# Performance work log

Hardware: AMD Instinct MI355X
Metric: run time of the kernel (lower is better)

Reference implementation:

```python
import jax, jax.numpy as jnp
import numpy as np

BATCH_BMM = 4      # opt.batch_size // len(opt.gpu_ids)
EPS = 1.0          # opt.eps (Sinkhorn entropic regularization)
MAX_ITER = 50
_STAB = 1e-8


def _cost_matrix_cos(x, y):
    # x: [B, n, d], y: [B, m, d] -> C = 1 - cosine similarity, [B, n, m]
    xn = x / (jnp.linalg.norm(x, axis=-1, keepdims=True) + _STAB)
    yn = y / (jnp.linalg.norm(y, axis=-1, keepdims=True) + _STAB)
    return 1.0 - jnp.einsum('bnd,bmd->bnm', xn, yn)


def _sinkhorn_plan(C, eps, max_iter):
    # Standard Sinkhorn with uniform marginals; returns transport plan pi [B, n, m]
    B, n, m = C.shape
    mu = jnp.full((B, n), 1.0 / n, dtype=C.dtype)
    nu = jnp.full((B, m), 1.0 / m, dtype=C.dtype)
    K = jnp.exp(-C / eps)  # Gibbs kernel, kept resident across iterations

    def body(carry, _):
        u, v = carry
        u = mu / (jnp.einsum('bnm,bm->bn', K, v) + _STAB)
        v = nu / (jnp.einsum('bnm,bn->bm', K, u) + _STAB)
        return (u, v), None

    (u, v), _ = jax.lax.scan(body, (jnp.ones_like(mu), jnp.ones_like(nu)),
                             None, length=max_iter)
    return u[:, :, None] * K * v[:, None, :]


def _OT(x, y, eps=EPS, max_iter=MAX_ITER):
    return _sinkhorn_plan(_cost_matrix_cos(x, y), eps, max_iter)


def setup_inputs() -> dict:
    key = jax.random.key(0)
    k1, k2, k3 = jax.random.split(key, 3)
    N, D = 8192, 256  # B*num_patches, feature dim
    return {
        'feat_src': jax.random.normal(k1, (N, D), dtype=jnp.float32),
        'feat_tgt': jax.random.normal(k2, (N, D), dtype=jnp.float32),
        'feat_gen': jax.random.normal(k3, (N, D), dtype=jnp.float32),
    }


def reference(feat_src, feat_tgt, feat_gen):
    dim = feat_src.shape[1]
    # .view(batch_dim_for_bmm, -1, dim); src/tgt are detached in the original
    ot_src = jax.lax.stop_gradient(feat_src.reshape(BATCH_BMM, -1, dim))
    ot_tgt = jax.lax.stop_gradient(feat_tgt.reshape(BATCH_BMM, -1, dim))
    ot_gen = feat_gen.reshape(BATCH_BMM, -1, dim)
    f1 = _OT(ot_src, ot_tgt)  # [B, n, n]
    f2 = _OT(ot_tgt, ot_gen)  # [B, n, n]
    return jnp.mean(jnp.abs(f1 - f2))  # F.l1_loss, reduction='mean'
```

## Files before the change

kernel.cpp:

```cpp
#include <hip/hip_runtime.h>
#include <math.h>

#define NP 2048
#define DF 256
#define NPROB 8
#define NTOT 8192

constexpr float F_MU   = 1.0f / 2048.0f;
constexpr float F_STAB = 1e-8f;

constexpr size_t OFF_K   = 0;
constexpr size_t SZ_K    = (size_t)NPROB * NP * NP;
constexpr size_t OFF_VA  = OFF_K + SZ_K;
constexpr size_t SZ_VA   = (size_t)3 * NPROB * NP;
constexpr size_t OFF_U   = OFF_VA + SZ_VA;
constexpr size_t SZ_U    = (size_t)NPROB * NP;
constexpr size_t OFF_INV = OFF_U + SZ_U;
constexpr size_t SZ_INV  = (size_t)3 * NTOT;
constexpr size_t OFF_SUM = OFF_INV + SZ_INV;

__global__ __launch_bounds__(256) void k_norms(const float* __restrict__ src,
                                               const float* __restrict__ tgt,
                                               const float* __restrict__ gen,
                                               float* __restrict__ inv) {
    int gw   = (blockIdx.x * 256 + threadIdx.x) >> 6;
    int lane = threadIdx.x & 63;
    int a = gw >> 13;
    int r = gw & 8191;
    const float* base = (a == 0 ? src : (a == 1 ? tgt : gen)) + (size_t)r * DF;
    float4 x = reinterpret_cast<const float4*>(base)[lane];
    float s = x.x * x.x + x.y * x.y + x.z * x.z + x.w * x.w;
    #pragma unroll
    for (int off = 32; off; off >>= 1) s += __shfl_xor(s, off);
    if (lane == 0) inv[gw] = 1.0f / (sqrtf(s) + F_STAB);
}

__global__ void k_init(float* __restrict__ va0, float* __restrict__ sum) {
    int i = blockIdx.x * 256 + threadIdx.x;
    if (i < NPROB * NP) va0[i] = 0.0f;
    if (i == 0) sum[0] = 0.0f;
}

#define TK 16
__global__ __launch_bounds__(256) void k_build(const float* __restrict__ src,
                                               const float* __restrict__ tgt,
                                               const float* __restrict__ gen,
                                               const float* __restrict__ inv,
                                               float* __restrict__ K) {
    __shared__ float As[128][TK + 1];
    __shared__ float Bs[128][TK + 1];
    int bid = blockIdx.x;
    int p   = bid >> 8;
    int t   = bid & 255;
    int ti  = t >> 4, tj = t & 15;
    int ot  = p >> 2, b = p & 3;
    const float* X    = (ot == 0) ? src : tgt;
    const float* Y    = (ot == 0) ? tgt : gen;
    const float* invx = inv + (ot == 0 ? 0 : NTOT);
    const float* invy = inv + (ot == 0 ? NTOT : 2 * NTOT);
    int rowA0 = b * NP + ti * 128;
    int rowB0 = b * NP + tj * 128;

    int tid = threadIdx.x;
    int ty  = tid >> 4, tx = tid & 15;

    float acc[8][8];
    #pragma unroll
    for (int i = 0; i < 8; ++i)
        #pragma unroll
        for (int j = 0; j < 8; ++j) acc[i][j] = 0.0f;

    for (int kb = 0; kb < DF; kb += TK) {
        __syncthreads();
        #pragma unroll
        for (int s = 0; s < 2; ++s) {
            int j4  = tid + s * 256;
            int row = j4 >> 2;
            int c4  = (j4 & 3) * 4;
            float4 av = *reinterpret_cast<const float4*>(X + (size_t)(rowA0 + row) * DF + kb + c4);
            float  sa = invx[rowA0 + row];
            As[row][c4 + 0] = av.x * sa; As[row][c4 + 1] = av.y * sa;
            As[row][c4 + 2] = av.z * sa; As[row][c4 + 3] = av.w * sa;
            float4 bv = *reinterpret_cast<const float4*>(Y + (size_t)(rowB0 + row) * DF + kb + c4);
            float  sb = invy[rowB0 + row];
            Bs[row][c4 + 0] = bv.x * sb; Bs[row][c4 + 1] = bv.y * sb;
            Bs[row][c4 + 2] = bv.z * sb; Bs[row][c4 + 3] = bv.w * sb;
        }
        __syncthreads();
        #pragma unroll
        for (int kk = 0; kk < TK; ++kk) {
            float a[8], bb[8];
            #pragma unroll
            for (int i = 0; i < 8; ++i) a[i]  = As[ty + 16 * i][kk];
            #pragma unroll
            for (int j = 0; j < 8; ++j) bb[j] = Bs[tx + 16 * j][kk];
            #pragma unroll
            for (int i = 0; i < 8; ++i)
                #pragma unroll
                for (int j = 0; j < 8; ++j) acc[i][j] += a[i] * bb[j];
        }
    }

    float* Kp = K + (size_t)p * NP * NP;
    #pragma unroll
    for (int i = 0; i < 8; ++i) {
        int gi = ti * 128 + ty + 16 * i;
        #pragma unroll
        for (int j = 0; j < 8; ++j) {
            int gj = tj * 128 + tx + 16 * j;
            Kp[(size_t)gi * NP + gj] = expf(acc[i][j] - 1.0f);
        }
    }
}

__global__ __launch_bounds__(256) void k_sink(const float* __restrict__ K,
                                              float* __restrict__ u,
                                              const float* __restrict__ vR,
                                              float* __restrict__ vW,
                                              float* __restrict__ vZ,
                                              int first) {
    __shared__ float lds[4][NP];
    int bid  = blockIdx.x;
    int p    = bid >> 6;
    int blk  = bid & 63;
    int tid  = threadIdx.x;
    int w    = tid >> 6, lane = tid & 63;

    if (tid < 32) vZ[bid * 32 + tid] = 0.0f;

    float4 vr[8];
    if (first) {
        #pragma unroll
        for (int c = 0; c < 8; ++c) vr[c] = make_float4(1.f, 1.f, 1.f, 1.f);
    } else {
        const float4* vRp = reinterpret_cast<const float4*>(vR + (size_t)p * NP);
        #pragma unroll
        for (int c = 0; c < 8; ++c) {
            float4 r4 = vRp[c * 64 + lane];
            vr[c] = make_float4(F_MU / (r4.x + F_STAB), F_MU / (r4.y + F_STAB),
                                F_MU / (r4.z + F_STAB), F_MU / (r4.w + F_STAB));
        }
    }

    const float* Kp = K + (size_t)p * NP * NP;
    float4 va[8];
    #pragma unroll
    for (int c = 0; c < 8; ++c) va[c] = make_float4(0.f, 0.f, 0.f, 0.f);

    int row0 = blk * 32 + w * 8;
    for (int r = 0; r < 8; ++r) {
        int row = row0 + r;
        const float4* krow = reinterpret_cast<const float4*>(Kp + (size_t)row * NP);
        float4 k4[8];
        #pragma unroll
        for (int c = 0; c < 8; ++c) k4[c] = krow[c * 64 + lane];
        float d = 0.f;
        #pragma unroll
        for (int c = 0; c < 8; ++c)
            d += k4[c].x * vr[c].x + k4[c].y * vr[c].y + k4[c].z * vr[c].z + k4[c].w * vr[c].w;
        #pragma unroll
        for (int off = 32; off; off >>= 1) d += __shfl_xor(d, off);
        float ui = F_MU / (d + F_STAB);
        if (lane == 0) u[p * NP + row] = ui;
        #pragma unroll
        for (int c = 0; c < 8; ++c) {
            va[c].x += k4[c].x * ui; va[c].y += k4[c].y * ui;
            va[c].z += k4[c].z * ui; va[c].w += k4[c].w * ui;
        }
    }

    float4* lw = reinterpret_cast<float4*>(lds[w]);
    #pragma unroll
    for (int c = 0; c < 8; ++c) lw[c * 64 + lane] = va[c];
    __syncthreads();
    float* vWp = vW + (size_t)p * NP;
    const float4* l0 = reinterpret_cast<const float4*>(lds[0]);
    const float4* l1 = reinterpret_cast<const float4*>(lds[1]);
    const float4* l2 = reinterpret_cast<const float4*>(lds[2]);
    const float4* l3 = reinterpret_cast<const float4*>(lds[3]);
    #pragma unroll
    for (int s = 0; s < 2; ++s) {
        int j = tid + s * 256;
        float4 a0 = l0[j], a1 = l1[j], a2 = l2[j], a3 = l3[j];
        atomicAdd(&vWp[4 * j + 0], a0.x + a1.x + a2.x + a3.x);
        atomicAdd(&vWp[4 * j + 1], a0.y + a1.y + a2.y + a3.y);
        atomicAdd(&vWp[4 * j + 2], a0.z + a1.z + a2.z + a3.z);
        atomicAdd(&vWp[4 * j + 3], a0.w + a1.w + a2.w + a3.w);
    }
}

__global__ __launch_bounds__(256) void k_freduce(const float* __restrict__ K,
                                                 const float* __restrict__ u,
                                                 const float* __restrict__ vF,
                                                 float* __restrict__ sum) {
    int bid = blockIdx.x;
    int b   = bid >> 6;
    int blk = bid & 63;
    int tid = threadIdx.x;
    int w   = tid >> 6, lane = tid & 63;
    int p1 = b, p2 = 4 + b;

    float4 v1[8], v2[8];
    const float4* vF1 = reinterpret_cast<const float4*>(vF + (size_t)p1 * NP);
    const float4* vF2 = reinterpret_cast<const float4*>(vF + (size_t)p2 * NP);
    #pragma unroll
    for (int c = 0; c < 8; ++c) {
        float4 r1 = vF1[c * 64 + lane], r2 = vF2[c * 64 + lane];
        v1[c] = make_float4(F_MU / (r1.x + F_STAB), F_MU / (r1.y + F_STAB),
                            F_MU / (r1.z + F_STAB), F_MU / (r1.w + F_STAB));
        v2[c] = make_float4(F_MU / (r2.x + F_STAB), F_MU / (r2.y + F_STAB),
                            F_MU / (r2.z + F_STAB), F_MU / (r2.w + F_STAB));
    }
    const float* K1 = K + (size_t)p1 * NP * NP;
    const float* K2 = K + (size_t)p2 * NP * NP;
    float acc = 0.f;
    int row0 = blk * 32 + w * 8;
    for (int r = 0; r < 8; ++r) {
        int row = row0 + r;
        float u1 = u[p1 * NP + row], u2 = u[p2 * NP + row];
        const float4* k1 = reinterpret_cast<const float4*>(K1 + (size_t)row * NP);
        const float4* k2 = reinterpret_cast<const float4*>(K2 + (size_t)row * NP);
        #pragma unroll
        for (int c = 0; c < 8; ++c) {
            float4 a = k1[c * 64 + lane], bb = k2[c * 64 + lane];
            acc += fabsf(u1 * a.x * v1[c].x - u2 * bb.x * v2[c].x);
            acc += fabsf(u1 * a.y * v1[c].y - u2 * bb.y * v2[c].y);
            acc += fabsf(u1 * a.z * v1[c].z - u2 * bb.z * v2[c].z);
            acc += fabsf(u1 * a.w * v1[c].w - u2 * bb.w * v2[c].w);
        }
    }
    #pragma unroll
    for (int off = 32; off; off >>= 1) acc += __shfl_xor(acc, off);
    __shared__ float red[4];
    if (lane == 0) red[w] = acc;
    __syncthreads();
    if (tid == 0) atomicAdd(sum, red[0] + red[1] + red[2] + red[3]);
}

__global__ void k_final(const float* __restrict__ sum, float* __restrict__ out) {
    out[0] = sum[0] * (1.0f / 16777216.0f);
}

extern "C" void kernel_launch(void* const* d_in, const int* in_sizes, int n_in,
                              void* d_out, int out_size, void* d_ws, size_t ws_size,
                              hipStream_t stream) {
    const float* src = (const float*)d_in[0];
    const float* tgt = (const float*)d_in[1];
    const float* gen = (const float*)d_in[2];
    float* ws  = (float*)d_ws;
    float* Kw  = ws + OFF_K;
    float* va  = ws + OFF_VA;
    float* uu  = ws + OFF_U;
    float* inv = ws + OFF_INV;
    float* sum = ws + OFF_SUM;
    float* out = (float*)d_out;

    hipLaunchKernelGGL(k_norms, dim3(6144), dim3(256), 0, stream, src, tgt, gen, inv);
    hipLaunchKernelGGL(k_init,  dim3(65),   dim3(256), 0, stream, va, sum);
    hipLaunchKernelGGL(k_build, dim3(2048), dim3(256), 0, stream, src, tgt, gen, inv, Kw);
    for (int t = 0; t < 50; ++t) {
        float* R = va + ((size_t)((t + 2) % 3)) * (NPROB * NP);
        float* W = va + ((size_t)(t % 3))       * (NPROB * NP);
        float* Z = va + ((size_t)((t + 1) % 3)) * (NPROB * NP);
        hipLaunchKernelGGL(k_sink, dim3(512), dim3(256), 0, stream,
                           Kw, uu, R, W, Z, (t == 0) ? 1 : 0);
    }
    hipLaunchKernelGGL(k_freduce, dim3(256), dim3(256), 0, stream,
                       Kw, uu, va + (size_t)1 * (NPROB * NP), sum);
    hipLaunchKernelGGL(k_final, dim3(1), dim3(1), 0, stream, sum, out);
}
```

Before: 2.040 ms.

## Store Gibbs kernel as 16-bit fixed-point to halve Sinkhorn memory traffic

The Gibbs kernel K is quantized to unsigned 16-bit fixed point (scaled by 65535) instead of stored as fp32, halving the bytes streamed on each of the 50 Sinkhorn iterations and in the final reduction. The sink and reduce kernels unpack the values on the fly, with the stabilizer epsilon rescaled to match. The grids are doubled with fewer rows per block, and the GEMM LDS reads are vectorized to float4. The quantization adds relative error to K, especially for small entries, which could shift the loss beyond tolerance.

```diff
diff --git a/kernel.cpp b/kernel.cpp
--- a/kernel.cpp
+++ b/kernel.cpp
@@ -6,18 +6,25 @@
 #define NPROB 8
 #define NTOT 8192
 
-constexpr float F_MU   = 1.0f / 2048.0f;
-constexpr float F_STAB = 1e-8f;
+constexpr float F_MU  = 1.0f / 2048.0f;
+constexpr float SQ    = 65535.0f;
+constexpr float EPS_U = 65535.0f * 1e-8f;
+constexpr float EPS_V = 1e-8f;
 
 constexpr size_t OFF_K   = 0;
-constexpr size_t SZ_K    = (size_t)NPROB * NP * NP;
-constexpr size_t OFF_VA  = OFF_K + SZ_K;
+constexpr size_t SZ_Kf   = (size_t)NPROB * NP * NP / 2;
+constexpr size_t OFF_VA  = OFF_K + SZ_Kf;
 constexpr size_t SZ_VA   = (size_t)3 * NPROB * NP;
 constexpr size_t OFF_U   = OFF_VA + SZ_VA;
 constexpr size_t SZ_U    = (size_t)NPROB * NP;
 constexpr size_t OFF_INV = OFF_U + SZ_U;
 constexpr size_t SZ_INV  = (size_t)3 * NTOT;
 constexpr size_t OFF_SUM = OFF_INV + SZ_INV;
+
+__device__ inline float4 unpack4(unsigned a, unsigned b) {
+    return make_float4((float)(a & 0xffffu), (float)(a >> 16),
+                       (float)(b & 0xffffu), (float)(b >> 16));
+}
 
 __global__ __launch_bounds__(256) void k_norms(const float* __restrict__ src,
                                                const float* __restrict__ tgt,
@@ -32,7 +39,7 @@
     float s = x.x * x.x + x.y * x.y + x.z * x.z + x.w * x.w;
     #pragma unroll
     for (int off = 32; off; off >>= 1) s += __shfl_xor(s, off);
-    if (lane == 0) inv[gw] = 1.0f / (sqrtf(s) + F_STAB);
+    if (lane == 0) inv[gw] = 1.0f / (sqrtf(s) + 1e-8f);
 }
 
 __global__ void k_init(float* __restrict__ va0, float* __restrict__ sum) {
@@ -42,13 +49,14 @@
 }
 
 #define TK 16
+#define TP 20
 __global__ __launch_bounds__(256) void k_build(const float* __restrict__ src,
                                                const float* __restrict__ tgt,
                                                const float* __restrict__ gen,
                                                const float* __restrict__ inv,
-                                               float* __restrict__ K) {
-    __shared__ float As[128][TK + 1];
-    __shared__ float Bs[128][TK + 1];
+                                               unsigned short* __restrict__ K) {
+    __shared__ float As[128][TP];
+    __shared__ float Bs[128][TP];
     int bid = blockIdx.x;
     int p   = bid >> 8;
     int t   = bid & 255;
@@ -79,154 +87,180 @@
             int c4  = (j4 & 3) * 4;
             float4 av = *reinterpret_cast<const float4*>(X + (size_t)(rowA0 + row) * DF + kb + c4);
             float  sa = invx[rowA0 + row];
-            As[row][c4 + 0] = av.x * sa; As[row][c4 + 1] = av.y * sa;
-            As[row][c4 + 2] = av.z * sa; As[row][c4 + 3] = av.w * sa;
+            av.x *= sa; av.y *= sa; av.z *= sa; av.w *= sa;
+            *reinterpret_cast<float4*>(&As[row][c4]) = av;
             float4 bv = *reinterpret_cast<const float4*>(Y + (size_t)(rowB0 + row) * DF + kb + c4);
             float  sb = invy[rowB0 + row];
-            Bs[row][c4 + 0] = bv.x * sb; Bs[row][c4 + 1] = bv.y * sb;
-            Bs[row][c4 + 2] = bv.z * sb; Bs[row][c4 + 3] = bv.w * sb;
+            bv.x *= sb; bv.y *= sb; bv.z *= sb; bv.w *= sb;
+            *reinterpret_cast<float4*>(&Bs[row][c4]) = bv;
         }
         __syncthreads();
         #pragma unroll
-        for (int kk = 0; kk < TK; ++kk) {
-            float a[8], bb[8];
+        for (int kk4 = 0; kk4 < TK; kk4 += 4) {
+            float4 a[8], bb[8];
             #pragma unroll
-            for (int i = 0; i < 8; ++i) a[i]  = As[ty + 16 * i][kk];
+            for (int i = 0; i < 8; ++i) a[i]  = *reinterpret_cast<const float4*>(&As[ty + 16 * i][kk4]);
             #pragma unroll
-            for (int j = 0; j < 8; ++j) bb[j] = Bs[tx + 16 * j][kk];
+            for (int j = 0; j < 8; ++j) bb[j] = *reinterpret_cast<const float4*>(&Bs[tx + 16 * j][kk4]);
             #pragma unroll
             for (int i = 0; i < 8; ++i)
                 #pragma unroll
-                for (int j = 0; j < 8; ++j) acc[i][j] += a[i] * bb[j];
-        }
-    }
-
-    float* Kp = K + (size_t)p * NP * NP;
+                for (int j = 0; j < 8; ++j)
+                    acc[i][j] += a[i].x * bb[j].x + a[i].y * bb[j].y
+                               + a[i].z * bb[j].z + a[i].w * bb[j].w;
+        }
+    }
+
+    unsigned short* Kp = K + (size_t)p * NP * NP;
     #pragma unroll
     for (int i = 0; i < 8; ++i) {
         int gi = ti * 128 + ty + 16 * i;
         #pragma unroll
         for (int j = 0; j < 8; ++j) {
             int gj = tj * 128 + tx + 16 * j;
-            Kp[(size_t)gi * NP + gj] = expf(acc[i][j] - 1.0f);
-        }
-    }
-}
-
-__global__ __launch_bounds__(256) void k_sink(const float* __restrict__ K,
-                                              float* __restrict__ u,
-                                              const float* __restrict__ vR,
-                                              float* __restrict__ vW,
-                                              float* __restrict__ vZ,
-                                              int first) {
-    __shared__ float lds[4][NP];
-    int bid  = blockIdx.x;
-    int p    = bid >> 6;
-    int blk  = bid & 63;
-    int tid  = threadIdx.x;
-    int w    = tid >> 6, lane = tid & 63;
-
-    if (tid < 32) vZ[bid * 32 + tid] = 0.0f;
-
-    float4 vr[8];
+            float k = expf(acc[i][j] - 1.0f);
+            Kp[(size_t)gi * NP + gj] = (unsigned short)__float2uint_rn(k * SQ);
+        }
+    }
+}
+
+__global__ __launch_bounds__(256, 4) void k_sink(const unsigned short* __restrict__ K,
+                                                 float* __restrict__ u,
+                                                 const float* __restrict__ vR,
+                                                 float* __restrict__ vW,
+                                                 float* __restrict__ vZ,
+                                                 int first) {
+    __shared__ float4 lds[4][512];
+    int bid = blockIdx.x;
+    int p   = bid >> 7;
+    int blk = bid & 127;
+    int tid = threadIdx.x;
+    int w   = tid >> 6, lane = tid & 63;
+
+    if (tid < 16) vZ[bid * 16 + tid] = 0.0f;
+
+    float vr[32];
     if (first) {
         #pragma unroll
-        for (int c = 0; c < 8; ++c) vr[c] = make_float4(1.f, 1.f, 1.f, 1.f);
+        for (int c = 0; c < 32; ++c) vr[c] = 1.0f;
     } else {
         const float4* vRp = reinterpret_cast<const float4*>(vR + (size_t)p * NP);
         #pragma unroll
-        for (int c = 0; c < 8; ++c) {
-            float4 r4 = vRp[c * 64 + lane];
-            vr[c] = make_float4(F_MU / (r4.x + F_STAB), F_MU / (r4.y + F_STAB),
-                                F_MU / (r4.z + F_STAB), F_MU / (r4.w + F_STAB));
-        }
-    }
-
-    const float* Kp = K + (size_t)p * NP * NP;
-    float4 va[8];
-    #pragma unroll
-    for (int c = 0; c < 8; ++c) va[c] = make_float4(0.f, 0.f, 0.f, 0.f);
-
-    int row0 = blk * 32 + w * 8;
-    for (int r = 0; r < 8; ++r) {
+        for (int j = 0; j < 4; ++j)
+            #pragma unroll
+            for (int h = 0; h < 2; ++h) {
+                float4 r = vRp[j * 128 + lane * 2 + h];
+                vr[j * 8 + h * 4 + 0] = F_MU / (r.x + EPS_V);
+                vr[j * 8 + h * 4 + 1] = F_MU / (r.y + EPS_V);
+                vr[j * 8 + h * 4 + 2] = F_MU / (r.z + EPS_V);
+                vr[j * 8 + h * 4 + 3] = F_MU / (r.w + EPS_V);
+            }
+    }
+
+    float va[32];
+    #pragma unroll
+    for (int c = 0; c < 32; ++c) va[c] = 0.0f;
+
+    const unsigned short* Kp = K + (size_t)p * NP * NP;
+    int row0 = blk * 16 + w * 4;
+    for (int r = 0; r < 4; ++r) {
         int row = row0 + r;
-        const float4* krow = reinterpret_cast<const float4*>(Kp + (size_t)row * NP);
-        float4 k4[8];
-        #pragma unroll
-        for (int c = 0; c < 8; ++c) k4[c] = krow[c * 64 + lane];
-        float d = 0.f;
-        #pragma unroll
-        for (int c = 0; c < 8; ++c)
-            d += k4[c].x * vr[c].x + k4[c].y * vr[c].y + k4[c].z * vr[c].z + k4[c].w * vr[c].w;
+        const uint4* kr = reinterpret_cast<const uint4*>(Kp + (size_t)row * NP);
+        uint4 q[4];
+        #pragma unroll
+        for (int j = 0; j < 4; ++j) q[j] = kr[j * 64 + lane];
+        float d = 0.0f;
+        #pragma unroll
+        for (int j = 0; j < 4; ++j) {
+            float4 f01 = unpack4(q[j].x, q[j].y);
+            float4 f23 = unpack4(q[j].z, q[j].w);
+            d += f01.x * vr[j*8+0] + f01.y * vr[j*8+1] + f01.z * vr[j*8+2] + f01.w * vr[j*8+3]
+               + f23.x * vr[j*8+4] + f23.y * vr[j*8+5] + f23.z * vr[j*8+6] + f23.w * vr[j*8+7];
+        }
         #pragma unroll
         for (int off = 32; off; off >>= 1) d += __shfl_xor(d, off);
-        float ui = F_MU / (d + F_STAB);
-        if (lane == 0) u[p * NP + row] = ui;
-        #pragma unroll
-        for (int c = 0; c < 8; ++c) {
-            va[c].x += k4[c].x * ui; va[c].y += k4[c].y * ui;
-            va[c].z += k4[c].z * ui; va[c].w += k4[c].w * ui;
-        }
-    }
-
-    float4* lw = reinterpret_cast<float4*>(lds[w]);
-    #pragma unroll
-    for (int c = 0; c < 8; ++c) lw[c * 64 + lane] = va[c];
+        float ui = F_MU / (d + EPS_U);
+        if (lane == 0) u[(size_t)p * NP + row] = ui;
+        #pragma unroll
+        for (int j = 0; j < 4; ++j) {
+            float4 f01 = unpack4(q[j].x, q[j].y);
+            float4 f23 = unpack4(q[j].z, q[j].w);
+            va[j*8+0] += f01.x * ui; va[j*8+1] += f01.y * ui;
+            va[j*8+2] += f01.z * ui; va[j*8+3] += f01.w * ui;
+            va[j*8+4] += f23.x * ui; va[j*8+5] += f23.y * ui;
+            va[j*8+6] += f23.z * ui; va[j*8+7] += f23.w * ui;
+        }
+    }
+
+    #pragma unroll
+    for (int j = 0; j < 4; ++j)
+        #pragma unroll
+        for (int h = 0; h < 2; ++h)
+            lds[w][(j * 2 + h) * 64 + lane] =
+                make_float4(va[j*8+h*4+0], va[j*8+h*4+1], va[j*8+h*4+2], va[j*8+h*4+3]);
     __syncthreads();
     float* vWp = vW + (size_t)p * NP;
-    const float4* l0 = reinterpret_cast<const float4*>(lds[0]);
-    const float4* l1 = reinterpret_cast<const float4*>(lds[1]);
-    const float4* l2 = reinterpret_cast<const float4*>(lds[2]);
-    const float4* l3 = reinterpret_cast<const float4*>(lds[3]);
     #pragma unroll
     for (int s = 0; s < 2; ++s) {
-        int j = tid + s * 256;
-        float4 a0 = l0[j], a1 = l1[j], a2 = l2[j], a3 = l3[j];
-        atomicAdd(&vWp[4 * j + 0], a0.x + a1.x + a2.x + a3.x);
-        atomicAdd(&vWp[4 * j + 1], a0.y + a1.y + a2.y + a3.y);
-        atomicAdd(&vWp[4 * j + 2], a0.z + a1.z + a2.z + a3.z);
-        atomicAdd(&vWp[4 * j + 3], a0.w + a1.w + a2.w + a3.w);
-    }
-}
-
-__global__ __launch_bounds__(256) void k_freduce(const float* __restrict__ K,
+        int pi = tid + s * 256;
+        int lr = pi & 63, hr = (pi >> 6) & 1, jr = pi >> 7;
+        int col4 = jr * 128 + lr * 2 + hr;
+        float4 a0 = lds[0][pi], a1 = lds[1][pi], a2 = lds[2][pi], a3 = lds[3][pi];
+        atomicAdd(&vWp[4 * col4 + 0], a0.x + a1.x + a2.x + a3.x);
+        atomicAdd(&vWp[4 * col4 + 1], a0.y + a1.y + a2.y + a3.y);
+        atomicAdd(&vWp[4 * col4 + 2], a0.z + a1.z + a2.z + a3.z);
+        atomicAdd(&vWp[4 * col4 + 3], a0.w + a1.w + a2.w + a3.w);
+    }
+}
+
+__global__ __launch_bounds__(256) void k_freduce(const unsigned short* __restrict__ K,
                                                  const float* __restrict__ u,
                                                  const float* __restrict__ vF,
                                                  float* __restrict__ sum) {
     int bid = blockIdx.x;
-    int b   = bid >> 6;
-    int blk = bid & 63;
+    int b   = bid >> 7;
+    int blk = bid & 127;
     int tid = threadIdx.x;
     int w   = tid >> 6, lane = tid & 63;
     int p1 = b, p2 = 4 + b;
 
-    float4 v1[8], v2[8];
+    float v1[32], v2[32];
     const float4* vF1 = reinterpret_cast<const float4*>(vF + (size_t)p1 * NP);
     const float4* vF2 = reinterpret_cast<const float4*>(vF + (size_t)p2 * NP);
     #pragma unroll
-    for (int c = 0; c < 8; ++c) {
-        float4 r1 = vF1[c * 64 + lane], r2 = vF2[c * 64 + lane];
-        v1[c] = make_float4(F_MU / (r1.x + F_STAB), F_MU / (r1.y + F_STAB),
-                            F_MU / (r1.z + F_STAB), F_MU / (r1.w + F_STAB));
-        v2[c] = make_float4(F_MU / (r2.x + F_STAB), F_MU / (r2.y + F_STAB),
-                            F_MU / (r2.z + F_STAB), F_MU / (r2.w + F_STAB));
-    }
-    const float* K1 = K + (size_t)p1 * NP * NP;
-    const float* K2 = K + (size_t)p2 * NP * NP;
-    float acc = 0.f;
-    int row0 = blk * 32 + w * 8;
-    for (int r = 0; r < 8; ++r) {
+    for (int j = 0; j < 4; ++j)
+        #pragma unroll
+        for (int h = 0; h < 2; ++h) {
+            float4 r1 = vF1[j * 128 + lane * 2 + h];
+            float4 r2 = vF2[j * 128 + lane * 2 + h];
+            v1[j*8+h*4+0] = F_MU / (r1.x + EPS_V); v1[j*8+h*4+1] = F_MU / (r1.y + EPS_V);
+            v1[j*8+h*4+2] = F_MU / (r1.z + EPS_V); v1[j*8+h*4+3] = F_MU / (r1.w + EPS_V);
+            v2[j*8+h*4+0] = F_MU / (r2.x + EPS_V); v2[j*8+h*4+1] = F_MU / (r2.y + EPS_V);
+            v2[j*8+h*4+2] = F_MU / (r2.z + EPS_V); v2[j*8+h*4+3] = F_MU / (r2.w + EPS_V);
+        }
+    const unsigned short* K1 = K + (size_t)p1 * NP * NP;
+    const unsigned short* K2 = K + (size_t)p2 * NP * NP;
+    float acc = 0.0f;
+    int row0 = blk * 16 + w * 4;
+    for (int r = 0; r < 4; ++r) {
         int row = row0 + r;
-        float u1 = u[p1 * NP + row], u2 = u[p2 * NP + row];
-        const float4* k1 = reinterpret_cast<const float4*>(K1 + (size_t)row * NP);
-        const float4* k2 = reinterpret_cast<const float4*>(K2 + (size_t)row * NP);
-        #pragma unroll
-        for (int c = 0; c < 8; ++c) {
-            float4 a = k1[c * 64 + lane], bb = k2[c * 64 + lane];
-            acc += fabsf(u1 * a.x * v1[c].x - u2 * bb.x * v2[c].x);
-            acc += fabsf(u1 * a.y * v1[c].y - u2 * bb.y * v2[c].y);
-            acc += fabsf(u1 * a.z * v1[c].z - u2 * bb.z * v2[c].z);
-            acc += fabsf(u1 * a.w * v1[c].w - u2 * bb.w * v2[c].w);
+        float u1 = u[(size_t)p1 * NP + row], u2 = u[(size_t)p2 * NP + row];
+        const uint4* kr1 = reinterpret_cast<const uint4*>(K1 + (size_t)row * NP);
+        const uint4* kr2 = reinterpret_cast<const uint4*>(K2 + (size_t)row * NP);
+        #pragma unroll
+        for (int j = 0; j < 4; ++j) {
+            uint4 q1 = kr1[j * 64 + lane];
+            uint4 q2 = kr2[j * 64 + lane];
+            float4 a01 = unpack4(q1.x, q1.y), a23 = unpack4(q1.z, q1.w);
+            float4 b01 = unpack4(q2.x, q2.y), b23 = unpack4(q2.z, q2.w);
+            acc += fabsf(u1 * a01.x * v1[j*8+0] - u2 * b01.x * v2[j*8+0]);
+            acc += fabsf(u1 * a01.y * v1[j*8+1] - u2 * b01.y * v2[j*8+1]);
+            acc += fabsf(u1 * a01.z * v1[j*8+2] - u2 * b01.z * v2[j*8+2]);
+            acc += fabsf(u1 * a01.w * v1[j*8+3] - u2 * b01.w * v2[j*8+3]);
+            acc += fabsf(u1 * a23.x * v1[j*8+4] - u2 * b23.x * v2[j*8+4]);
+            acc += fabsf(u1 * a23.y * v1[j*8+5] - u2 * b23.y * v2[j*8+5]);
+            acc += fabsf(u1 * a23.z * v1[j*8+6] - u2 * b23.z * v2[j*8+6]);
+            acc += fabsf(u1 * a23.w * v1[j*8+7] - u2 * b23.w * v2[j*8+7]);
         }
     }
     #pragma unroll
@@ -248,7 +282,7 @@
     const float* tgt = (const float*)d_in[1];
     const float* gen = (const float*)d_in[2];
     float* ws  = (float*)d_ws;
-    float* Kw  = ws + OFF_K;
+    unsigned short* Kq = (unsigned short*)(ws + OFF_K);
     float* va  = ws + OFF_VA;
     float* uu  = ws + OFF_U;
     float* inv = ws + OFF_INV;
@@ -257,15 +291,15 @@
 
     hipLaunchKernelGGL(k_norms, dim3(6144), dim3(256), 0, stream, src, tgt, gen, inv);
     hipLaunchKernelGGL(k_init,  dim3(65),   dim3(256), 0, stream, va, sum);
-    hipLaunchKernelGGL(k_build, dim3(2048), dim3(256), 0, stream, src, tgt, gen, inv, Kw);
+    hipLaunchKernelGGL(k_build, dim3(2048), dim3(256), 0, stream, src, tgt, gen, inv, Kq);
     for (int t = 0; t < 50; ++t) {
         float* R = va + ((size_t)((t + 2) % 3)) * (NPROB * NP);
         float* W = va + ((size_t)(t % 3))       * (NPROB * NP);
         float* Z = va + ((size_t)((t + 1) % 3)) * (NPROB * NP);
-        hipLaunchKernelGGL(k_sink, dim3(512), dim3(256), 0, stream,
-                           Kw, uu, R, W, Z, (t == 0) ? 1 : 0);
-    }
-    hipLaunchKernelGGL(k_freduce, dim3(256), dim3(256), 0, stream,
-                       Kw, uu, va + (size_t)1 * (NPROB * NP), sum);
+        hipLaunchKernelGGL(k_sink, dim3(1024), dim3(256), 0, stream,
+                           Kq, uu, R, W, Z, (t == 0) ? 1 : 0);
+    }
+    hipLaunchKernelGGL(k_freduce, dim3(512), dim3(256), 0, stream,
+                       Kq, uu, va + (size_t)1 * (NPROB * NP), sum);
     hipLaunchKernelGGL(k_final, dim3(1), dim3(1), 0, stream, sum, out);
 }
```

Result: slower. 5.390 ms (+164.2%).
